# Kernel tuning notes

Hardware: AMD Instinct MI355X
Metric: run time of the kernel (lower is better)

Reference implementation:

```python
import jax, jax.numpy as jnp
import numpy as np

B, F, D = 32768, 2668, 64

def _xn(key, shape):
    # xavier_normal_: std = sqrt(2/(fan_in+fan_out))
    std = np.sqrt(2.0 / (shape[0] + shape[1]))
    return jax.random.normal(key, shape, dtype=jnp.float32) * std

def setup_inputs() -> dict:
    key = jax.random.key(0)
    ks = jax.random.split(key, 16)
    fv = jax.random.uniform(ks[0], (B, F), dtype=jnp.float32)
    sizes = [(1, 'age_user_w'), (1, 'age_item_w'), (2, 'gender_user_w'), (2, 'gender_item_w'),
             (21, 'occupation_user_w'), (21, 'occupation_item_w'), (19, 'movie_user_w'), (19, 'movie_item_w'),
             (943, 'userid_user_w'), (943, 'userid_item_w'), (1682, 'itemid_user_w'), (1682, 'itemid_item_w')]
    inp = {'feature_vector': fv}
    for i, (n, name) in enumerate(sizes):
        inp[name] = _xn(ks[i + 1], (n, D))
    # nn.Linear(F,1): kaiming-uniform weight, uniform bias; plain uniform scale suffices for a reference
    bound = 1.0 / np.sqrt(F)
    inp['lin_w'] = jax.random.uniform(ks[13], (1, F), dtype=jnp.float32, minval=-bound, maxval=bound)
    inp['lin_b'] = jax.random.uniform(ks[14], (1,), dtype=jnp.float32, minval=-bound, maxval=bound)
    return inp

def reference(feature_vector, age_user_w, age_item_w, gender_user_w, gender_item_w,
              occupation_user_w, occupation_item_w, movie_user_w, movie_item_w,
              userid_user_w, userid_item_w, itemid_user_w, itemid_item_w, lin_w, lin_b):
    fv = feature_vector
    au = fv[:, 2626:2627] @ age_user_w          # [B, D] (note: column 2626 reused, as in source)
    ai = fv[:, 2626:2627] @ age_item_w
    gu = fv[:, 2626:2628] @ gender_user_w
    gi = fv[:, 2626:2628] @ gender_item_w
    ou = fv[:, 2628:2649] @ occupation_user_w
    oi = fv[:, 2628:2649] @ occupation_item_w
    mu = fv[:, 2649:2668] @ movie_user_w
    mi = fv[:, 2649:2668] @ movie_item_w
    uu = fv[:, 0:943] @ userid_user_w
    ui = fv[:, 0:943] @ userid_item_w
    tu = fv[:, 943:2625] @ itemid_user_w
    ti = fv[:, 943:2625] @ itemid_item_w
    cross = jnp.sum(au * gu + au * ou + ai * mu + au * uu + ai * tu
                    + gu * ou + gi * mu + gu * uu + gi * tu
                    + oi * mu + ou * uu + oi * tu
                    + mu * ui + mi * ti + ui * tu, axis=1)   # [B]
    logits = fv @ lin_w.T + lin_b + cross[:, None]           # [B, 1]
    return jax.nn.sigmoid(logits)
```

## Files before the change

### kernel.cpp

```cpp
#include <hip/hip_runtime.h>

#define FDIM 2668

typedef float f32x4 __attribute__((ext_vector_type(4)));
typedef _Float16 f16x8 __attribute__((ext_vector_type(8)));

#define G1_NK 30
#define G2_NK 54
#define G3_NK 2
#define G1_NT 9
#define G2_NT 9
#define G3_NT 29
#define G1_NS 15
#define G2_NS 27

#define HU 0
#define HT (G1_NK * G1_NT * 512)
#define HS (HT + G2_NK * G2_NT * 512)
#define H_TOTAL (HS + G3_NK * G3_NT * 512)

#define SUPB (G1_NT * 2048)
#define LDSB (4 * SUPB)

__global__ __launch_bounds__(256) void ffm_prep(
    const float* __restrict__ au_, const float* __restrict__ ai_,
    const float* __restrict__ gu_, const float* __restrict__ gi_,
    const float* __restrict__ ou_, const float* __restrict__ oi_,
    const float* __restrict__ mu_, const float* __restrict__ mi_,
    const float* __restrict__ uu_, const float* __restrict__ ui_,
    const float* __restrict__ tu_, const float* __restrict__ ti_,
    const float* __restrict__ lw, _Float16* __restrict__ ws) {
  int e = blockIdx.x * 256 + threadIdx.x;
  if (e >= H_TOTAL) return;
  float val = 0.f;
  int rel, ntiles;
  if (e < HT) { rel = e; ntiles = G1_NT; }
  else if (e < HS) { rel = e - HT; ntiles = G2_NT; }
  else { rel = e - HS; ntiles = G3_NT; }
  int perk = ntiles * 512;
  int kb = rel / perk;
  int r = rel - kb * perk;
  int nt = r >> 9; r &= 511;
  int lane = r >> 3, j = r & 7;
  int k = kb * 32 + ((lane >> 4) << 3) + j;
  int n = (nt << 4) + (lane & 15);

  if (e < HT) {
    if (k < 943) {
      if (n < 64) val = uu_[k * 64 + n];
      else if (n < 128) val = ui_[k * 64 + n - 64];
      else if (n == 128) val = lw[k];
    }
  } else if (e < HS) {
    int col = 940 + k;
    if (n < 64) { if (col >= 943 && col < 2625) val = tu_[(col - 943) * 64 + n]; }
    else if (n < 128) { if (col >= 943 && col < 2625) val = ti_[(col - 943) * 64 + n - 64]; }
    else if (n == 128) { if (col >= 943 && col <= 2635) val = lw[col]; }
  } else {
    int col = 2624 + k;
    if (n == 448) { if (col >= 2636 && col < 2668) val = lw[col]; }
    else if (n < 448) {
      int blk = n >> 6, d = n & 63;
      float ageu = (col == 2626) ? au_[d] : 0.f;
      float agei = (col == 2626) ? ai_[d] : 0.f;
      float genu = (col >= 2626 && col < 2628) ? gu_[(col - 2626) * 64 + d] : 0.f;
      float geni = (col >= 2626 && col < 2628) ? gi_[(col - 2626) * 64 + d] : 0.f;
      float occu = (col >= 2628 && col < 2649) ? ou_[(col - 2628) * 64 + d] : 0.f;
      float occi = (col >= 2628 && col < 2649) ? oi_[(col - 2628) * 64 + d] : 0.f;
      float movu = (col >= 2649 && col < 2668) ? mu_[(col - 2649) * 64 + d] : 0.f;
      float movi = (col >= 2649 && col < 2668) ? mi_[(col - 2649) * 64 + d] : 0.f;
      switch (blk) {
        case 0: val = ageu + genu + occu; break;
        case 1: val = agei + geni + occi; break;
        case 2: val = movu; break;
        case 3: val = movi; break;
        case 4: val = ageu; break;
        case 5: val = genu; break;
        case 6: val = occu; break;
      }
    }
  }
  ws[e] = (_Float16)val;
}

__device__ __forceinline__ void gll16(const _Float16* __restrict__ src, char* dst) {
  __builtin_amdgcn_global_load_lds((const __attribute__((address_space(1))) void*)src,
                                   (__attribute__((address_space(3))) void*)dst, 16, 0, 0);
}

template <int NT>
__device__ __forceinline__ void stageS(const _Float16* __restrict__ src, char* lds,
                                       int bufOff, int tid, int wave) {
  constexpr int chunks = NT * 128;
#pragma unroll
  for (int base = 0; base < chunks; base += 256) {
    int idx = base + tid;
    if (idx < chunks)
      gll16(src + (size_t)idx * 8, lds + bufOff + (base + wave * 64) * 16);
  }
}

__device__ __forceinline__ void loadS(f32x4 (&A)[4], const float* __restrict__ myrow, int cs) {
  A[0] = *(const f32x4*)(myrow + cs);
  A[1] = *(const f32x4*)(myrow + cs + 4);
  A[2] = *(const f32x4*)(myrow + cs + 32);
  A[3] = *(const f32x4*)(myrow + cs + 36);
}

template <bool GUARD>
__device__ __forceinline__ f32x4 ldg4(const float* __restrict__ myrow, int c) {
  f32x4 z = {0.f, 0.f, 0.f, 0.f};
  if (!GUARD || (c + 4) <= FDIM) return *(const f32x4*)(myrow + c);
  return z;
}

__device__ __forceinline__ void syncw(int sel, bool hiw) {
  if (sel == 2) {
    if (hiw) asm volatile("s_waitcnt vmcnt(14) lgkmcnt(0)" ::: "memory");
    else     asm volatile("s_waitcnt vmcnt(12) lgkmcnt(0)" ::: "memory");
  } else if (sel == 1) {
    if (hiw) asm volatile("s_waitcnt vmcnt(9) lgkmcnt(0)" ::: "memory");
    else     asm volatile("s_waitcnt vmcnt(8) lgkmcnt(0)" ::: "memory");
  } else {
    asm volatile("s_waitcnt vmcnt(0) lgkmcnt(0)" ::: "memory");
  }
  __builtin_amdgcn_s_barrier();
}

template <int NT, int NS>
__device__ __forceinline__ void pbody(int k, f32x4 (&Au)[4], f32x4 (&An)[4],
                                      const float* __restrict__ myrow, int colbase,
                                      const _Float16* __restrict__ wsrc, char* lds,
                                      int tid, int lane, int kg, int wave, bool hiw,
                                      f32x4* acc) {
  int sel = (k + 2 < NS) ? 2 : ((k + 1 < NS) ? 1 : 0);
  syncw(sel, hiw);
  if (k + 2 < NS) loadS(An, myrow, colbase + (k + 2) * 64 + kg * 8);
  if (k + 3 < NS)
    stageS<NT>(wsrc + (size_t)(k + 3) * (NT * 1024), lds, ((k + 3) & 3) * SUPB, tid, wave);
  f16x8 af0, af1;
#pragma unroll
  for (int i = 0; i < 4; ++i) {
    af0[i] = (_Float16)Au[0][i]; af0[4 + i] = (_Float16)Au[1][i];
    af1[i] = (_Float16)Au[2][i]; af1[4 + i] = (_Float16)Au[3][i];
  }
  const char* buf = lds + ((k & 3) * SUPB) + lane * 16;
#pragma unroll
  for (int nt = 0; nt < NT; ++nt)
    acc[nt] = __builtin_amdgcn_mfma_f32_16x16x32_f16(
        af0, *(const f16x8*)(buf + nt * 1024), acc[nt], 0, 0, 0);
#pragma unroll
  for (int nt = 0; nt < NT; ++nt)
    acc[nt] = __builtin_amdgcn_mfma_f32_16x16x32_f16(
        af1, *(const f16x8*)(buf + NT * 1024 + nt * 1024), acc[nt], 0, 0, 0);
}

template <int NT, int NS>
__device__ __forceinline__ void phaseP(const float* __restrict__ myrow, int colbase,
                                       const _Float16* __restrict__ wsrc, char* lds,
                                       int tid, int lane, int kg, int wave, bool hiw,
                                       f32x4* acc) {
  static_assert(NS % 3 == 0, "NS must be divisible by 3 for static A rotation");
  f32x4 A0[4], A1[4], A2[4];
  stageS<NT>(wsrc, lds, 0, tid, wave);
  loadS(A0, myrow, colbase + kg * 8);
  stageS<NT>(wsrc + (size_t)(NT * 1024), lds, SUPB, tid, wave);
  loadS(A1, myrow, colbase + 64 + kg * 8);
  stageS<NT>(wsrc + (size_t)2 * (NT * 1024), lds, 2 * SUPB, tid, wave);
  for (int kb = 0; kb < NS; kb += 3) {
    pbody<NT, NS>(kb + 0, A0, A2, myrow, colbase, wsrc, lds, tid, lane, kg, wave, hiw, acc);
    pbody<NT, NS>(kb + 1, A1, A0, myrow, colbase, wsrc, lds, tid, lane, kg, wave, hiw, acc);
    pbody<NT, NS>(kb + 2, A2, A1, myrow, colbase, wsrc, lds, tid, lane, kg, wave, hiw, acc);
  }
}

__global__ __launch_bounds__(256, 2) void ffm_main(
    const float* __restrict__ fv, const _Float16* __restrict__ wp,
    const float* __restrict__ linb, float* __restrict__ out) {
  __shared__ __align__(16) char lds[LDSB];
  const int tid = threadIdx.x;
  const int lane = tid & 63;
  const int wave = tid >> 6;
  const int nl = lane & 15;
  const int kg = lane >> 4;
  const bool hiw = tid < 128;
  const int rowbase = blockIdx.x * 64 + wave * 16;
  const float* myrow = fv + (size_t)(rowbase + nl) * FDIM;
  const f32x4 zero4 = {0.f, 0.f, 0.f, 0.f};

  f32x4 s[G3_NT];
#pragma unroll
  for (int i = 0; i < G3_NT; ++i) s[i] = zero4;
  {
    constexpr int chunks = G3_NT * 64 * G3_NK;
#pragma unroll
    for (int base = 0; base < chunks; base += 256) {
      int idx = base + tid;
      if (idx < chunks)
        gll16(wp + HS + (size_t)idx * 8, lds + (base + wave * 64) * 16);
    }
    f32x4 a0 = ldg4<true>(myrow, 2624 + kg * 8);
    f32x4 a1 = ldg4<true>(myrow, 2624 + kg * 8 + 4);
    f32x4 a2 = ldg4<true>(myrow, 2656 + kg * 8);
    f32x4 a3 = ldg4<true>(myrow, 2656 + kg * 8 + 4);
    asm volatile("s_waitcnt vmcnt(0) lgkmcnt(0)" ::: "memory");
    __builtin_amdgcn_s_barrier();
    f16x8 af0, af1;
#pragma unroll
    for (int i = 0; i < 4; ++i) {
      af0[i] = (_Float16)a0[i]; af0[4 + i] = (_Float16)a1[i];
      af1[i] = (_Float16)a2[i]; af1[4 + i] = (_Float16)a3[i];
    }
    const char* buf = lds + lane * 16;
#pragma unroll
    for (int nt = 0; nt < G3_NT; ++nt)
      s[nt] = __builtin_amdgcn_mfma_f32_16x16x32_f16(
          af0, *(const f16x8*)(buf + nt * 1024), s[nt], 0, 0, 0);
#pragma unroll
    for (int nt = 0; nt < G3_NT; ++nt)
      s[nt] = __builtin_amdgcn_mfma_f32_16x16x32_f16(
          af1, *(const f16x8*)(buf + G3_NT * 1024 + nt * 1024), s[nt], 0, 0, 0);
    asm volatile("s_waitcnt lgkmcnt(0)" ::: "memory");
    __builtin_amdgcn_s_barrier();
  }

  f32x4 P[4], Q[4], MU[4], MI[4];
  f32x4 cross = s[28];
#pragma unroll
  for (int t = 0; t < 4; ++t) {
    P[t] = s[t]; Q[t] = s[4 + t]; MU[t] = s[8 + t]; MI[t] = s[12 + t];
    cross += s[16 + t] * (s[20 + t] + s[24 + t]) + s[20 + t] * s[24 + t] + MU[t] * Q[t];
  }

  f32x4 u[G1_NT];
#pragma unroll
  for (int i = 0; i < G1_NT; ++i) u[i] = zero4;
  phaseP<G1_NT, G1_NS>(myrow, 0, wp + HU, lds, tid, lane, kg, wave, hiw, u);
  cross += u[8];
#pragma unroll
  for (int t = 0; t < 4; ++t) {
    cross += u[t] * P[t] + u[4 + t] * MU[t];
    Q[t] += u[4 + t];
  }
  asm volatile("s_waitcnt lgkmcnt(0)" ::: "memory");
  __builtin_amdgcn_s_barrier();

  f32x4 v[G2_NT];
#pragma unroll
  for (int i = 0; i < G2_NT; ++i) v[i] = zero4;
  phaseP<G2_NT, G2_NS>(myrow, 940, wp + HT, lds, tid, lane, kg, wave, hiw, v);
  cross += v[8];
#pragma unroll
  for (int t = 0; t < 4; ++t)
    cross += v[t] * Q[t] + v[4 + t] * MI[t];

  float c0 = cross[0], c1 = cross[1], c2 = cross[2], c3 = cross[3];
#pragma unroll
  for (int m = 1; m <= 8; m <<= 1) {
    c0 += __shfl_xor(c0, m, 64);
    c1 += __shfl_xor(c1, m, 64);
    c2 += __shfl_xor(c2, m, 64);
    c3 += __shfl_xor(c3, m, 64);
  }
  if (nl == 0) {
    float lb = linb[0];
    int r = rowbase + kg * 4;
    out[r + 0] = 1.f / (1.f + __expf(-(c0 + lb)));
    out[r + 1] = 1.f / (1.f + __expf(-(c1 + lb)));
    out[r + 2] = 1.f / (1.f + __expf(-(c2 + lb)));
    out[r + 3] = 1.f / (1.f + __expf(-(c3 + lb)));
  }
}

extern "C" void kernel_launch(void* const* d_in, const int* in_sizes, int n_in,
                              void* d_out, int out_size, void* d_ws, size_t ws_size,
                              hipStream_t stream) {
  const float* fv    = (const float*)d_in[0];
  const float* age_u = (const float*)d_in[1];
  const float* age_i = (const float*)d_in[2];
  const float* gen_u = (const float*)d_in[3];
  const float* gen_i = (const float*)d_in[4];
  const float* occ_u = (const float*)d_in[5];
  const float* occ_i = (const float*)d_in[6];
  const float* mov_u = (const float*)d_in[7];
  const float* mov_i = (const float*)d_in[8];
  const float* uid_u = (const float*)d_in[9];
  const float* uid_i = (const float*)d_in[10];
  const float* iid_u = (const float*)d_in[11];
  const float* iid_i = (const float*)d_in[12];
  const float* lin_w = (const float*)d_in[13];
  const float* lin_b = (const float*)d_in[14];
  _Float16* ws = (_Float16*)d_ws;
  float* out = (float*)d_out;

  ffm_prep<<<(H_TOTAL + 255) / 256, 256, 0, stream>>>(
      age_u, age_i, gen_u, gen_i, occ_u, occ_i, mov_u, mov_i,
      uid_u, uid_i, iid_u, iid_i, lin_w, ws);
  ffm_main<<<32768 / 64, 256, 0, stream>>>(fv, ws, lin_b, out);
}
```

Baseline: 505.6 us.

## Give each wave two 16-row M tiles to reuse B fragments across rows

Blocks shrink from four waves to two, and each wave now computes two 16-row tiles. Every B fragment read from LDS feeds two MFMAs, which halves LDS traffic per row and removes the per-wave vmcnt selection. The cost is twice the accumulator and A-register pressure, and occupancy changes with launch bounds of (128,1). Staging loops become guard-free with 128-thread strides.

```diff
diff --git a/kernel.cpp b/kernel.cpp
--- a/kernel.cpp
+++ b/kernel.cpp
@@ -92,19 +92,24 @@
 __device__ __forceinline__ void stageS(const _Float16* __restrict__ src, char* lds,
                                        int bufOff, int tid, int wave) {
   constexpr int chunks = NT * 128;
-#pragma unroll
-  for (int base = 0; base < chunks; base += 256) {
+  static_assert(chunks % 128 == 0, "guard-free staging requires chunks %% 128 == 0");
+#pragma unroll
+  for (int base = 0; base < chunks; base += 128) {
     int idx = base + tid;
-    if (idx < chunks)
-      gll16(src + (size_t)idx * 8, lds + bufOff + (base + wave * 64) * 16);
-  }
-}
-
-__device__ __forceinline__ void loadS(f32x4 (&A)[4], const float* __restrict__ myrow, int cs) {
-  A[0] = *(const f32x4*)(myrow + cs);
-  A[1] = *(const f32x4*)(myrow + cs + 4);
-  A[2] = *(const f32x4*)(myrow + cs + 32);
-  A[3] = *(const f32x4*)(myrow + cs + 36);
+    gll16(src + (size_t)idx * 8, lds + bufOff + (base + wave * 64) * 16);
+  }
+}
+
+__device__ __forceinline__ void loadS2(f32x4 (&A)[8], const float* __restrict__ r0,
+                                       const float* __restrict__ r1, int cs) {
+  A[0] = *(const f32x4*)(r0 + cs);
+  A[1] = *(const f32x4*)(r0 + cs + 4);
+  A[2] = *(const f32x4*)(r0 + cs + 32);
+  A[3] = *(const f32x4*)(r0 + cs + 36);
+  A[4] = *(const f32x4*)(r1 + cs);
+  A[5] = *(const f32x4*)(r1 + cs + 4);
+  A[6] = *(const f32x4*)(r1 + cs + 32);
+  A[7] = *(const f32x4*)(r1 + cs + 36);
 }
 
 template <bool GUARD>
@@ -114,67 +119,65 @@
   return z;
 }
 
-__device__ __forceinline__ void syncw(int sel, bool hiw) {
-  if (sel == 2) {
-    if (hiw) asm volatile("s_waitcnt vmcnt(14) lgkmcnt(0)" ::: "memory");
-    else     asm volatile("s_waitcnt vmcnt(12) lgkmcnt(0)" ::: "memory");
-  } else if (sel == 1) {
-    if (hiw) asm volatile("s_waitcnt vmcnt(9) lgkmcnt(0)" ::: "memory");
-    else     asm volatile("s_waitcnt vmcnt(8) lgkmcnt(0)" ::: "memory");
-  } else {
-    asm volatile("s_waitcnt vmcnt(0) lgkmcnt(0)" ::: "memory");
-  }
+template <int NT, int NS>
+__device__ __forceinline__ void pbody(int k, f32x4 (&Au)[8], f32x4 (&An)[8],
+                                      const float* __restrict__ r0,
+                                      const float* __restrict__ r1, int colbase,
+                                      const _Float16* __restrict__ wsrc, char* lds,
+                                      int tid, int lane, int kg, int wave,
+                                      f32x4 (&acc0)[NT], f32x4 (&acc1)[NT]) {
+  if (k < NS - 1) asm volatile("s_waitcnt vmcnt(17) lgkmcnt(0)" ::: "memory");
+  else            asm volatile("s_waitcnt vmcnt(0) lgkmcnt(0)" ::: "memory");
   __builtin_amdgcn_s_barrier();
-}
-
-template <int NT, int NS>
-__device__ __forceinline__ void pbody(int k, f32x4 (&Au)[4], f32x4 (&An)[4],
-                                      const float* __restrict__ myrow, int colbase,
-                                      const _Float16* __restrict__ wsrc, char* lds,
-                                      int tid, int lane, int kg, int wave, bool hiw,
-                                      f32x4* acc) {
-  int sel = (k + 2 < NS) ? 2 : ((k + 1 < NS) ? 1 : 0);
-  syncw(sel, hiw);
-  if (k + 2 < NS) loadS(An, myrow, colbase + (k + 2) * 64 + kg * 8);
+  if (k + 2 < NS) loadS2(An, r0, r1, colbase + (k + 2) * 64 + kg * 8);
   if (k + 3 < NS)
     stageS<NT>(wsrc + (size_t)(k + 3) * (NT * 1024), lds, ((k + 3) & 3) * SUPB, tid, wave);
-  f16x8 af0, af1;
+  f16x8 a00, a01, a10, a11;
 #pragma unroll
   for (int i = 0; i < 4; ++i) {
-    af0[i] = (_Float16)Au[0][i]; af0[4 + i] = (_Float16)Au[1][i];
-    af1[i] = (_Float16)Au[2][i]; af1[4 + i] = (_Float16)Au[3][i];
+    a00[i] = (_Float16)Au[0][i]; a00[4 + i] = (_Float16)Au[1][i];
+    a01[i] = (_Float16)Au[2][i]; a01[4 + i] = (_Float16)Au[3][i];
+    a10[i] = (_Float16)Au[4][i]; a10[4 + i] = (_Float16)Au[5][i];
+    a11[i] = (_Float16)Au[6][i]; a11[4 + i] = (_Float16)Au[7][i];
   }
   const char* buf = lds + ((k & 3) * SUPB) + lane * 16;
 #pragma unroll
-  for (int nt = 0; nt < NT; ++nt)
-    acc[nt] = __builtin_amdgcn_mfma_f32_16x16x32_f16(
-        af0, *(const f16x8*)(buf + nt * 1024), acc[nt], 0, 0, 0);
-#pragma unroll
-  for (int nt = 0; nt < NT; ++nt)
-    acc[nt] = __builtin_amdgcn_mfma_f32_16x16x32_f16(
-        af1, *(const f16x8*)(buf + NT * 1024 + nt * 1024), acc[nt], 0, 0, 0);
+  for (int nt = 0; nt < NT; ++nt) {
+    f16x8 b0 = *(const f16x8*)(buf + nt * 1024);
+    acc0[nt] = __builtin_amdgcn_mfma_f32_16x16x32_f16(a00, b0, acc0[nt], 0, 0, 0);
+    acc1[nt] = __builtin_amdgcn_mfma_f32_16x16x32_f16(a10, b0, acc1[nt], 0, 0, 0);
+  }
+#pragma unroll
+  for (int nt = 0; nt < NT; ++nt) {
+    f16x8 b1 = *(const f16x8*)(buf + NT * 1024 + nt * 1024);
+    acc0[nt] = __builtin_amdgcn_mfma_f32_16x16x32_f16(a01, b1, acc0[nt], 0, 0, 0);
+    acc1[nt] = __builtin_amdgcn_mfma_f32_16x16x32_f16(a11, b1, acc1[nt], 0, 0, 0);
+  }
 }
 
 template <int NT, int NS>
-__device__ __forceinline__ void phaseP(const float* __restrict__ myrow, int colbase,
+__device__ __forceinline__ void phaseP(const float* __restrict__ r0,
+                                       const float* __restrict__ r1, int colbase,
                                        const _Float16* __restrict__ wsrc, char* lds,
-                                       int tid, int lane, int kg, int wave, bool hiw,
-                                       f32x4* acc) {
+                                       int tid, int lane, int kg, int wave,
+                                       f32x4 (&acc0)[NT], f32x4 (&acc1)[NT]) {
   static_assert(NS % 3 == 0, "NS must be divisible by 3 for static A rotation");
-  f32x4 A0[4], A1[4], A2[4];
+  f32x4 A0[8], A1[8], A2[8];
   stageS<NT>(wsrc, lds, 0, tid, wave);
-  loadS(A0, myrow, colbase + kg * 8);
+  loadS2(A0, r0, r1, colbase + kg * 8);
+  asm volatile("" ::: "memory");
   stageS<NT>(wsrc + (size_t)(NT * 1024), lds, SUPB, tid, wave);
-  loadS(A1, myrow, colbase + 64 + kg * 8);
+  loadS2(A1, r0, r1, colbase + 64 + kg * 8);
+  asm volatile("" ::: "memory");
   stageS<NT>(wsrc + (size_t)2 * (NT * 1024), lds, 2 * SUPB, tid, wave);
   for (int kb = 0; kb < NS; kb += 3) {
-    pbody<NT, NS>(kb + 0, A0, A2, myrow, colbase, wsrc, lds, tid, lane, kg, wave, hiw, acc);
-    pbody<NT, NS>(kb + 1, A1, A0, myrow, colbase, wsrc, lds, tid, lane, kg, wave, hiw, acc);
-    pbody<NT, NS>(kb + 2, A2, A1, myrow, colbase, wsrc, lds, tid, lane, kg, wave, hiw, acc);
-  }
-}
-
-__global__ __launch_bounds__(256, 2) void ffm_main(
+    pbody<NT, NS>(kb + 0, A0, A2, r0, r1, colbase, wsrc, lds, tid, lane, kg, wave, acc0, acc1);
+    pbody<NT, NS>(kb + 1, A1, A0, r0, r1, colbase, wsrc, lds, tid, lane, kg, wave, acc0, acc1);
+    pbody<NT, NS>(kb + 2, A2, A1, r0, r1, colbase, wsrc, lds, tid, lane, kg, wave, acc0, acc1);
+  }
+}
+
+__global__ __launch_bounds__(128, 1) void ffm_main(
     const float* __restrict__ fv, const _Float16* __restrict__ wp,
     const float* __restrict__ linb, float* __restrict__ out) {
   __shared__ __align__(16) char lds[LDSB];
@@ -183,92 +186,121 @@
   const int wave = tid >> 6;
   const int nl = lane & 15;
   const int kg = lane >> 4;
-  const bool hiw = tid < 128;
-  const int rowbase = blockIdx.x * 64 + wave * 16;
-  const float* myrow = fv + (size_t)(rowbase + nl) * FDIM;
+  const int base = blockIdx.x * 64 + wave * 32;
+  const float* r0 = fv + (size_t)(base + nl) * FDIM;
+  const float* r1 = fv + (size_t)(base + 16 + nl) * FDIM;
   const f32x4 zero4 = {0.f, 0.f, 0.f, 0.f};
 
-  f32x4 s[G3_NT];
-#pragma unroll
-  for (int i = 0; i < G3_NT; ++i) s[i] = zero4;
+  f32x4 s0[G3_NT], s1[G3_NT];
+#pragma unroll
+  for (int i = 0; i < G3_NT; ++i) { s0[i] = zero4; s1[i] = zero4; }
   {
     constexpr int chunks = G3_NT * 64 * G3_NK;
-#pragma unroll
-    for (int base = 0; base < chunks; base += 256) {
-      int idx = base + tid;
-      if (idx < chunks)
-        gll16(wp + HS + (size_t)idx * 8, lds + (base + wave * 64) * 16);
-    }
-    f32x4 a0 = ldg4<true>(myrow, 2624 + kg * 8);
-    f32x4 a1 = ldg4<true>(myrow, 2624 + kg * 8 + 4);
-    f32x4 a2 = ldg4<true>(myrow, 2656 + kg * 8);
-    f32x4 a3 = ldg4<true>(myrow, 2656 + kg * 8 + 4);
+    static_assert(chunks % 128 == 0, "G3 staging must be guard-free");
+#pragma unroll
+    for (int b = 0; b < chunks; b += 128) {
+      int idx = b + tid;
+      gll16(wp + HS + (size_t)idx * 8, lds + (b + wave * 64) * 16);
+    }
+    f32x4 a[8];
+    a[0] = ldg4<false>(r0, 2624 + kg * 8);
+    a[1] = ldg4<false>(r0, 2628 + kg * 8);
+    a[2] = ldg4<true>(r0, 2656 + kg * 8);
+    a[3] = ldg4<true>(r0, 2660 + kg * 8);
+    a[4] = ldg4<false>(r1, 2624 + kg * 8);
+    a[5] = ldg4<false>(r1, 2628 + kg * 8);
+    a[6] = ldg4<true>(r1, 2656 + kg * 8);
+    a[7] = ldg4<true>(r1, 2660 + kg * 8);
     asm volatile("s_waitcnt vmcnt(0) lgkmcnt(0)" ::: "memory");
     __builtin_amdgcn_s_barrier();
-    f16x8 af0, af1;
+    f16x8 a00, a01, a10, a11;
 #pragma unroll
     for (int i = 0; i < 4; ++i) {
-      af0[i] = (_Float16)a0[i]; af0[4 + i] = (_Float16)a1[i];
-      af1[i] = (_Float16)a2[i]; af1[4 + i] = (_Float16)a3[i];
+      a00[i] = (_Float16)a[0][i]; a00[4 + i] = (_Float16)a[1][i];
+      a01[i] = (_Float16)a[2][i]; a01[4 + i] = (_Float16)a[3][i];
+      a10[i] = (_Float16)a[4][i]; a10[4 + i] = (_Float16)a[5][i];
+      a11[i] = (_Float16)a[6][i]; a11[4 + i] = (_Float16)a[7][i];
     }
     const char* buf = lds + lane * 16;
 #pragma unroll
-    for (int nt = 0; nt < G3_NT; ++nt)
-      s[nt] = __builtin_amdgcn_mfma_f32_16x16x32_f16(
-          af0, *(const f16x8*)(buf + nt * 1024), s[nt], 0, 0, 0);
-#pragma unroll
-    for (int nt = 0; nt < G3_NT; ++nt)
-      s[nt] = __builtin_amdgcn_mfma_f32_16x16x32_f16(
-          af1, *(const f16x8*)(buf + G3_NT * 1024 + nt * 1024), s[nt], 0, 0, 0);
+    for (int nt = 0; nt < G3_NT; ++nt) {
+      f16x8 b0 = *(const f16x8*)(buf + nt * 1024);
+      s0[nt] = __builtin_amdgcn_mfma_f32_16x16x32_f16(a00, b0, s0[nt], 0, 0, 0);
+      s1[nt] = __builtin_amdgcn_mfma_f32_16x16x32_f16(a10, b0, s1[nt], 0, 0, 0);
+    }
+#pragma unroll
+    for (int nt = 0; nt < G3_NT; ++nt) {
+      f16x8 b1 = *(const f16x8*)(buf + G3_NT * 1024 + nt * 1024);
+      s0[nt] = __builtin_amdgcn_mfma_f32_16x16x32_f16(a01, b1, s0[nt], 0, 0, 0);
+      s1[nt] = __builtin_amdgcn_mfma_f32_16x16x32_f16(a11, b1, s1[nt], 0, 0, 0);
+    }
     asm volatile("s_waitcnt lgkmcnt(0)" ::: "memory");
     __builtin_amdgcn_s_barrier();
   }
 
-  f32x4 P[4], Q[4], MU[4], MI[4];
-  f32x4 cross = s[28];
+  f32x4 P[2][4], Q[2][4], MU[2][4], MI[2][4], cross[2];
+  cross[0] = s0[28]; cross[1] = s1[28];
 #pragma unroll
   for (int t = 0; t < 4; ++t) {
-    P[t] = s[t]; Q[t] = s[4 + t]; MU[t] = s[8 + t]; MI[t] = s[12 + t];
-    cross += s[16 + t] * (s[20 + t] + s[24 + t]) + s[20 + t] * s[24 + t] + MU[t] * Q[t];
-  }
-
-  f32x4 u[G1_NT];
-#pragma unroll
-  for (int i = 0; i < G1_NT; ++i) u[i] = zero4;
-  phaseP<G1_NT, G1_NS>(myrow, 0, wp + HU, lds, tid, lane, kg, wave, hiw, u);
-  cross += u[8];
+    P[0][t] = s0[t]; Q[0][t] = s0[4 + t]; MU[0][t] = s0[8 + t]; MI[0][t] = s0[12 + t];
+    cross[0] += s0[16 + t] * (s0[20 + t] + s0[24 + t]) + s0[20 + t] * s0[24 + t]
+                + MU[0][t] * Q[0][t];
+    P[1][t] = s1[t]; Q[1][t] = s1[4 + t]; MU[1][t] = s1[8 + t]; MI[1][t] = s1[12 + t];
+    cross[1] += s1[16 + t] * (s1[20 + t] + s1[24 + t]) + s1[20 + t] * s1[24 + t]
+                + MU[1][t] * Q[1][t];
+  }
+
+  f32x4 u0[G1_NT], u1[G1_NT];
+#pragma unroll
+  for (int i = 0; i < G1_NT; ++i) { u0[i] = zero4; u1[i] = zero4; }
+  phaseP<G1_NT, G1_NS>(r0, r1, 0, wp + HU, lds, tid, lane, kg, wave, u0, u1);
+  cross[0] += u0[8]; cross[1] += u1[8];
 #pragma unroll
   for (int t = 0; t < 4; ++t) {
-    cross += u[t] * P[t] + u[4 + t] * MU[t];
-    Q[t] += u[4 + t];
+    cross[0] += u0[t] * P[0][t] + u0[4 + t] * MU[0][t];
+    Q[0][t] += u0[4 + t];
+    cross[1] += u1[t] * P[1][t] + u1[4 + t] * MU[1][t];
+    Q[1][t] += u1[4 + t];
   }
   asm volatile("s_waitcnt lgkmcnt(0)" ::: "memory");
   __builtin_amdgcn_s_barrier();
 
-  f32x4 v[G2_NT];
-#pragma unroll
-  for (int i = 0; i < G2_NT; ++i) v[i] = zero4;
-  phaseP<G2_NT, G2_NS>(myrow, 940, wp + HT, lds, tid, lane, kg, wave, hiw, v);
-  cross += v[8];
-#pragma unroll
-  for (int t = 0; t < 4; ++t)
-    cross += v[t] * Q[t] + v[4 + t] * MI[t];
-
-  float c0 = cross[0], c1 = cross[1], c2 = cross[2], c3 = cross[3];
+  f32x4 v0[G2_NT], v1[G2_NT];
+#pragma unroll
+  for (int i = 0; i < G2_NT; ++i) { v0[i] = zero4; v1[i] = zero4; }
+  phaseP<G2_NT, G2_NS>(r0, r1, 940, wp + HT, lds, tid, lane, kg, wave, v0, v1);
+  cross[0] += v0[8]; cross[1] += v1[8];
+#pragma unroll
+  for (int t = 0; t < 4; ++t) {
+    cross[0] += v0[t] * Q[0][t] + v0[4 + t] * MI[0][t];
+    cross[1] += v1[t] * Q[1][t] + v1[4 + t] * MI[1][t];
+  }
+
+  float c0 = cross[0][0], c1 = cross[0][1], c2 = cross[0][2], c3 = cross[0][3];
+  float c4 = cross[1][0], c5 = cross[1][1], c6 = cross[1][2], c7 = cross[1][3];
 #pragma unroll
   for (int m = 1; m <= 8; m <<= 1) {
     c0 += __shfl_xor(c0, m, 64);
     c1 += __shfl_xor(c1, m, 64);
     c2 += __shfl_xor(c2, m, 64);
     c3 += __shfl_xor(c3, m, 64);
+    c4 += __shfl_xor(c4, m, 64);
+    c5 += __shfl_xor(c5, m, 64);
+    c6 += __shfl_xor(c6, m, 64);
+    c7 += __shfl_xor(c7, m, 64);
   }
   if (nl == 0) {
     float lb = linb[0];
-    int r = rowbase + kg * 4;
-    out[r + 0] = 1.f / (1.f + __expf(-(c0 + lb)));
-    out[r + 1] = 1.f / (1.f + __expf(-(c1 + lb)));
-    out[r + 2] = 1.f / (1.f + __expf(-(c2 + lb)));
-    out[r + 3] = 1.f / (1.f + __expf(-(c3 + lb)));
+    int ra = base + kg * 4;
+    out[ra + 0] = 1.f / (1.f + __expf(-(c0 + lb)));
+    out[ra + 1] = 1.f / (1.f + __expf(-(c1 + lb)));
+    out[ra + 2] = 1.f / (1.f + __expf(-(c2 + lb)));
+    out[ra + 3] = 1.f / (1.f + __expf(-(c3 + lb)));
+    int rb = base + 16 + kg * 4;
+    out[rb + 0] = 1.f / (1.f + __expf(-(c4 + lb)));
+    out[rb + 1] = 1.f / (1.f + __expf(-(c5 + lb)));
+    out[rb + 2] = 1.f / (1.f + __expf(-(c6 + lb)));
+    out[rb + 3] = 1.f / (1.f + __expf(-(c7 + lb)));
   }
 }
 
@@ -296,5 +328,5 @@
   ffm_prep<<<(H_TOTAL + 255) / 256, 256, 0, stream>>>(
       age_u, age_i, gen_u, gen_i, occ_u, occ_i, mov_u, mov_i,
       uid_u, uid_i, iid_u, iid_i, lin_w, ws);
-  ffm_main<<<32768 / 64, 256, 0, stream>>>(fv, ws, lin_b, out);
-}
+  ffm_main<<<32768 / 64, 128, 0, stream>>>(fv, ws, lin_b, out);
+}
```

Result: no change. 507.3 us (+0.3%).
